# Optimization experiments

Hardware: AMD Instinct MI355X
Metric: run time of the kernel (lower is better)

Reference implementation:

```python
import jax, jax.numpy as jnp
import numpy as np
from jax import lax

EPS = 1e-5
S_CENTROIDS = 2048
K_NEIGH = 32


def _fps(xyz, S):
    """Farthest point sampling. xyz: (B,N,3) -> idx (B,S) int32."""
    B, N, _ = xyz.shape

    def body(carry, _):
        dist, farthest = carry  # (B,N), (B,)
        centroid = jnp.take_along_axis(xyz, farthest[:, None, None], axis=1)  # (B,1,3)
        d = jnp.sum((xyz - centroid) ** 2, axis=-1)  # (B,N)
        dist = jnp.minimum(dist, d)
        nxt = jnp.argmax(dist, axis=-1).astype(jnp.int32)
        return (dist, nxt), farthest

    init = (jnp.full((B, N), 1e10, xyz.dtype), jnp.zeros((B,), jnp.int32))
    _, idx = lax.scan(body, init, None, length=S)
    return idx.T  # (B,S)


def _knn(q, p, K):
    """q: (B,S,3) queries, p: (B,N,3) points -> idx (B,S,K) of K nearest."""
    d = (jnp.sum(q * q, -1)[:, :, None] + jnp.sum(p * p, -1)[:, None, :]
         - 2.0 * jnp.einsum('bsd,bnd->bsn', q, p))  # (B,S,N) sq dists
    _, idx = lax.top_k(-d, K)
    return idx


def _mlp_layer(x, w, g, b, m, v):
    # x: (B,S,K,Cin); 1x1 conv == channel matmul, then eval-mode BN, then ReLU
    x = jnp.einsum('bskc,oc->bsko', x, w)
    x = (x - m) * (g * lax.rsqrt(v + EPS)) + b
    return jax.nn.relu(x)


def setup_inputs() -> dict:
    key = jax.random.key(0)
    ks = jax.random.split(key, 8)
    B, N, D = 4, 8192, 64
    inp = {
        'xyz': jax.random.normal(ks[0], (B, N, 3), jnp.float32),
        'points': jax.random.normal(ks[1], (B, D, N), jnp.float32),
        'w0': jax.random.normal(ks[2], (64, 67), jnp.float32) * (1.0 / np.sqrt(67)),
        'g0': jnp.ones((64,), jnp.float32), 'b0': jnp.zeros((64,), jnp.float32),
        'm0': jnp.zeros((64,), jnp.float32), 'v0': jnp.ones((64,), jnp.float32),
        'w1': jax.random.normal(ks[3], (64, 64), jnp.float32) * (1.0 / np.sqrt(64)),
        'g1': jnp.ones((64,), jnp.float32), 'b1': jnp.zeros((64,), jnp.float32),
        'm1': jnp.zeros((64,), jnp.float32), 'v1': jnp.ones((64,), jnp.float32),
        'w2': jax.random.normal(ks[4], (128, 64), jnp.float32) * (1.0 / np.sqrt(64)),
        'g2': jnp.ones((128,), jnp.float32), 'b2': jnp.zeros((128,), jnp.float32),
        'm2': jnp.zeros((128,), jnp.float32), 'v2': jnp.ones((128,), jnp.float32),
    }
    return inp


def reference(xyz, points, w0, g0, b0, m0, v0, w1, g1, b1, m1, v1,
              w2, g2, b2, m2, v2):
    B, N, _ = xyz.shape
    S, K = S_CENTROIDS, K_NEIGH

    # FPS centroids (S < N path of the module)
    fps_idx = _fps(xyz, S)                                        # (B,S)
    new_xyz = jnp.take_along_axis(xyz, fps_idx[..., None], axis=1)  # (B,S,3)

    # KNN grouping
    idx = _knn(new_xyz, xyz, K)                                   # (B,S,K)
    grouped_xyz = jnp.take_along_axis(xyz[:, None], idx[..., None], axis=2)  # (B,S,K,3)
    grouped_xyz = grouped_xyz - new_xyz[:, :, None, :]

    # gather neighbor features: points (B,D,N) -> (B,N,D) -> (B,S,K,D)
    pts = jnp.transpose(points, (0, 2, 1))
    neigh = jnp.take_along_axis(pts[:, None], idx[..., None], axis=2)
    grouped = jnp.concatenate([grouped_xyz, neigh], axis=-1)      # (B,S,K,3+D)

    x = _mlp_layer(grouped, w0, g0, b0, m0, v0)
    x = _mlp_layer(x, w1, g1, b1, m1, v1)
    x = _mlp_layer(x, w2, g2, b2, m2, v2)                         # (B,S,K,128)

    new_points = jnp.transpose(jnp.max(x, axis=2), (0, 2, 1))     # (B,128,S)
    return new_xyz, new_points
```

## Files before the change

### kernel.cpp

```cpp
#include <hip/hip_runtime.h>
#include <cfloat>
#include <climits>

#define NPTS   8192
#define SCENT  2048
#define KNEIGH 32
#define BATCH  4
#define DFEAT  64
#define FPS_T  512
#define NV     8
#define NW     8
#define CAP    64
#define NCONS  252
#define CPB    63

typedef float v2f __attribute__((ext_vector_type(2)));

#define DPPMAX(u, ctrl, rmask)                                                        \
    { unsigned _t = (unsigned)__builtin_amdgcn_update_dpp(0, (int)(u), (ctrl),        \
                                                          (rmask), 0xf, false);      \
      (u) = ((u) > _t) ? (u) : _t; }

struct FpsSh {
    float sx[NPTS], sy[NPTS], sz[NPTS];
    float hx[SCENT], hy[SCENT], hz[SCENT];
    alignas(16) unsigned slotV[2][NW];
    alignas(16) unsigned slotM[2][NW];
    int scand[CAP];
    int scnt;
    alignas(8) double sdd[2][NW];
    double sfv[NW];
    int sfo[NW];
};
struct ConsSh {
    float  spx[2048], spy[2048], spz[2048];
    double sp2[2048];
    float  tile[32 * 33];
    float  regA[64 * 68];
    float  regB[64 * 64];
    float  regC[128 * 64];
    float  prm[512];
};
union ShU { FpsSh f; ConsSh c; };

__global__ __launch_bounds__(FPS_T, 1) void fused_kernel(
        const float* __restrict__ xyz, float* __restrict__ new_xyz,
        const float* __restrict__ pts, float* __restrict__ ptsT,
        int* __restrict__ progress, int* __restrict__ tcount,
        float* __restrict__ out_points,
        const float* __restrict__ w0, const float* __restrict__ g0,
        const float* __restrict__ b0, const float* __restrict__ m0,
        const float* __restrict__ v0, const float* __restrict__ w1,
        const float* __restrict__ g1, const float* __restrict__ b1,
        const float* __restrict__ m1, const float* __restrict__ v1,
        const float* __restrict__ w2, const float* __restrict__ g2,
        const float* __restrict__ b2, const float* __restrict__ m2,
        const float* __restrict__ v2) {
    __shared__ ShU sh;
    const int t = threadIdx.x;
    const int lane = t & 63, w = t >> 6;

    if (blockIdx.x < BATCH) {
        FpsSh& S = sh.f;
        const int b = blockIdx.x;
        const float* X = xyz + (size_t)b * NPTS * 3;

        for (int p = t; p < NPTS; p += FPS_T) {
            S.sx[p] = X[3 * p + 0]; S.sy[p] = X[3 * p + 1]; S.sz[p] = X[3 * p + 2];
        }

        v2f px2[NV], py2[NV], pz2[NV], dist2[NV];
#pragma unroll
        for (int j = 0; j < NV; ++j) {
            int pA = t + FPS_T * j, pB = t + FPS_T * (j + NV);
            px2[j] = (v2f){X[3 * pA + 0], X[3 * pB + 0]};
            py2[j] = (v2f){X[3 * pA + 1], X[3 * pB + 1]};
            pz2[j] = (v2f){X[3 * pA + 2], X[3 * pB + 2]};
            dist2[j] = (v2f){1e10f, 1e10f};
        }
        float cx = X[0], cy = X[1], cz = X[2];
        int buf = 0;
        __syncthreads();

#pragma unroll 1
        for (int s = 0; s < SCENT; ++s) {
            if (t == 0) { S.hx[s] = cx; S.hy[s] = cy; S.hz[s] = cz; }

            const v2f cxx = {cx, cx}, cyy = {cy, cy}, czz = {cz, cz};
            v2f m2 = {-1.f, -1.f}, s2 = {-1.f, -1.f};
#pragma unroll
            for (int j = 0; j < NV; ++j) {
                v2f dx = px2[j] - cxx;
                v2f dy = py2[j] - cyy;
                v2f dz = pz2[j] - czz;
                v2f d  = __builtin_elementwise_fma(dx, dx,
                         __builtin_elementwise_fma(dy, dy, dz * dz));
                v2f nd = __builtin_elementwise_min(dist2[j], d);
                dist2[j] = nd;
                v2f lo = __builtin_elementwise_min(m2, nd);
                s2 = __builtin_elementwise_max(s2, lo);
                m2 = __builtin_elementwise_max(m2, nd);
            }
            const float m   = fmaxf(m2.x, m2.y);
            const float sec = fmaxf(fmaxf(s2.x, s2.y), fminf(m2.x, m2.y));

            int mi = 0;
#pragma unroll
            for (int j = 0; j < NV; ++j) {
                mi = (dist2[j].x == m) ? (t + FPS_T * j)        : mi;
                mi = (dist2[j].y == m) ? (t + FPS_T * (j + NV)) : mi;
            }

            unsigned myU = __float_as_uint(m);
            unsigned u = myU;
            DPPMAX(u, 0x111, 0xf);
            DPPMAX(u, 0x112, 0xf);
            DPPMAX(u, 0x114, 0xf);
            DPPMAX(u, 0x118, 0xf);
            DPPMAX(u, 0x142, 0xa);
            DPPMAX(u, 0x143, 0xc);
            const unsigned wu = (unsigned)__builtin_amdgcn_readlane((int)u, 63);

            unsigned long long wb = __ballot(myU == wu);
            const int wl   = __ffsll(wb) - 1;
            const int widx = __builtin_amdgcn_readlane(mi, wl);
            const float thwf = __fmul_rn(__uint_as_float(wu), 0.999998f);
            unsigned long long b1m = __ballot(m >= thwf);
            unsigned long long b2m = __ballot(sec >= thwf);
            const unsigned tw = (b2m || __popcll(b1m) >= 2) ? 1u : 0u;
            if (lane == 0) {
                S.slotV[buf][w] = wu;
                S.slotM[buf][w] = (unsigned)widx | (tw << 14);
            }
            __syncthreads();

            unsigned sv[NW], sm[NW];
            {
                const uint4* vp = (const uint4*)&S.slotV[buf][0];
                const uint4* mp = (const uint4*)&S.slotM[buf][0];
                uint4 a = vp[0], c = vp[1], e = mp[0], f = mp[1];
                sv[0] = a.x; sv[1] = a.y; sv[2] = a.z; sv[3] = a.w;
                sv[4] = c.x; sv[5] = c.y; sv[6] = c.z; sv[7] = c.w;
                sm[0] = e.x; sm[1] = e.y; sm[2] = e.z; sm[3] = e.w;
                sm[4] = f.x; sm[5] = f.y; sm[6] = f.z; sm[7] = f.w;
            }
            unsigned gu = sv[0];
#pragma unroll
            for (int k = 1; k < NW; ++k) gu = (sv[k] > gu) ? sv[k] : gu;
            const float gvf  = __uint_as_float(gu);
            const float gthf = __fmul_rn(gvf, 0.999998f);
            const unsigned ugth = __float_as_uint(gthf);
            int nw = 0; unsigned meta = 0;
#pragma unroll
            for (int k = NW - 1; k >= 0; --k) {
                nw += (sv[k] >= ugth) ? 1 : 0;
                meta = (sv[k] == gu) ? sm[k] : meta;
            }
            const int wtie = (meta >> 14) & 1;
            int i1 = (int)(meta & 0x3fffu);

            if (nw >= 2 || wtie) {
                if (t == 0) S.scnt = 0;
                __syncthreads();
#pragma unroll
                for (int j = 0; j < NV; ++j) {
                    if (dist2[j].x >= gthf) {
                        int slot = atomicAdd(&S.scnt, 1);
                        if (slot < CAP) S.scand[slot] = t + FPS_T * j;
                    }
                    if (dist2[j].y >= gthf) {
                        int slot = atomicAdd(&S.scnt, 1);
                        if (slot < CAP) S.scand[slot] = t + FPS_T * (j + NV);
                    }
                }
                __syncthreads();
                const int mm = S.scnt;
                if (mm <= CAP) {
                    double bd = -1.0; int bi = INT_MAX;
#pragma unroll 1
                    for (int k = 0; k < mm; ++k) {
                        const int pos = S.scand[k];
                        const double pxd = (double)S.sx[pos], pyd = (double)S.sy[pos],
                                     pzd = (double)S.sz[pos];
                        double dd = 1e10;
                        for (int i = t; i <= s; i += FPS_T) {
                            double ddx = __dsub_rn(pxd, (double)S.hx[i]);
                            double ddy = __dsub_rn(pyd, (double)S.hy[i]);
                            double ddz = __dsub_rn(pzd, (double)S.hz[i]);
                            double d = __dadd_rn(__dadd_rn(__dmul_rn(ddx, ddx), __dmul_rn(ddy, ddy)),
                                                 __dmul_rn(ddz, ddz));
                            dd = fmin(dd, d);
                        }
#pragma unroll
                        for (int off = 32; off >= 1; off >>= 1)
                            dd = fmin(dd, __shfl_down(dd, off));
                        if (lane == 0) S.sdd[k & 1][w] = dd;
                        __syncthreads();
                        double ddm = S.sdd[k & 1][0];
#pragma unroll
                        for (int w2i = 1; w2i < NW; ++w2i) ddm = fmin(ddm, S.sdd[k & 1][w2i]);
                        if (ddm > bd || (ddm == bd && pos < bi)) { bd = ddm; bi = pos; }
                    }
                    i1 = bi;
                } else {
                    double bv = -1.0; int bi = INT_MAX;
#pragma unroll 1
                    for (int j = 0; j < 2 * NV; ++j) {
                        const int jj = j & (NV - 1);
                        const bool hiHalf = j >= NV;
                        const double pxd = (double)(hiHalf ? px2[jj].y : px2[jj].x);
                        const double pyd = (double)(hiHalf ? py2[jj].y : py2[jj].x);
                        const double pzd = (double)(hiHalf ? pz2[jj].y : pz2[jj].x);
                        double dd = 1e10;
                        for (int i = 0; i <= s; ++i) {
                            double ddx = __dsub_rn(pxd, (double)S.hx[i]);
                            double ddy = __dsub_rn(pyd, (double)S.hy[i]);
                            double ddz = __dsub_rn(pzd, (double)S.hz[i]);
                            double d = __dadd_rn(__dadd_rn(__dmul_rn(ddx, ddx), __dmul_rn(ddy, ddy)),
                                                 __dmul_rn(ddz, ddz));
                            dd = fmin(dd, d);
                        }
                        int pidx = t + FPS_T * j;
                        if (dd > bv || (dd == bv && pidx < bi)) { bv = dd; bi = pidx; }
                    }
#pragma unroll
                    for (int off = 32; off >= 1; off >>= 1) {
                        double ov = __shfl_down(bv, off);
                        int    oi = __shfl_down(bi, off);
                        if (ov > bv || (ov == bv && oi < bi)) { bv = ov; bi = oi; }
                    }
                    if (lane == 0) { S.sfv[w] = bv; S.sfo[w] = bi; }
                    __syncthreads();
                    bv = S.sfv[0]; bi = S.sfo[0];
#pragma unroll
                    for (int w2i = 1; w2i < NW; ++w2i) {
                        double ov = S.sfv[w2i]; int oi = S.sfo[w2i];
                        if (ov > bv || (ov == bv && oi < bi)) { bv = ov; bi = oi; }
                    }
                    i1 = bi;
                }
                __syncthreads();
            }
            cx = S.sx[i1]; cy = S.sy[i1]; cz = S.sz[i1];

            if ((s & 63) == 63) {
                const int base0 = s - 63;
                if (t < 64 * 3) {
                    int ci = base0 + t / 3;
                    int cmp = t - (t / 3) * 3;
                    float v = (cmp == 0) ? S.hx[ci] : ((cmp == 1) ? S.hy[ci] : S.hz[ci]);
                    __hip_atomic_store(&new_xyz[((size_t)b * SCENT + base0) * 3 + t], v,
                                       __ATOMIC_RELAXED, __HIP_MEMORY_SCOPE_AGENT);
                }
                __syncthreads();
                if (t == 0)
                    __hip_atomic_store(&progress[b], s + 1,
                                       __ATOMIC_RELEASE, __HIP_MEMORY_SCOPE_AGENT);
            }
            buf ^= 1;
        }
    } else {
        ConsSh& K = sh.c;
        const int local = blockIdx.x - BATCH;
        const int batch = local / CPB;
        const int cl    = local % CPB;
        const int tx = t & 31, ty = t >> 5;

        for (int tid2 = local; tid2 < 2048; tid2 += NCONS) {
            const int bt = tid2 >> 9, rest = tid2 & 511;
            const int d0 = (rest >> 8) * 32, n0 = (rest & 255) * 32;
            __syncthreads();
#pragma unroll
            for (int i = 0; i < 2; ++i)
                K.tile[(ty + 16 * i) * 33 + tx] =
                    pts[(size_t)bt * DFEAT * NPTS + (size_t)(d0 + ty + 16 * i) * NPTS + n0 + tx];
            __syncthreads();
#pragma unroll
            for (int i = 0; i < 2; ++i)
                ptsT[(size_t)bt * NPTS * DFEAT + (size_t)(n0 + ty + 16 * i) * DFEAT + d0 + tx] =
                    K.tile[tx * 33 + ty + 16 * i];
        }
        if (t == 0) {
            __threadfence();
            atomicAdd(tcount, 1);
        }

        for (int idx = t; idx < 64 * 68; idx += FPS_T) {
            int o = idx / 68, i = idx - o * 68;
            float v;
            if (i < 64)      v = w0[o * 67 + 3 + i];
            else if (i < 67) v = w0[o * 67 + (i - 64)];
            else             v = 0.0f;
            K.regA[idx] = v;
        }
        for (int idx = t; idx < 64 * 64; idx += FPS_T)  K.regB[idx] = w1[idx];
        for (int idx = t; idx < 128 * 64; idx += FPS_T) K.regC[idx] = w2[idx];
        if (t < 64) {
            float a0v = g0[t] / sqrtf(v0[t] + 1e-5f);
            K.prm[t]       = a0v;
            K.prm[64 + t]  = b0[t] - m0[t] * a0v;
            float a1v = g1[t] / sqrtf(v1[t] + 1e-5f);
            K.prm[128 + t] = a1v;
            K.prm[192 + t] = b1[t] - m1[t] * a1v;
        } else if (t < 192) {
            int o = t - 64;
            float a2v = g2[o] / sqrtf(v2[o] + 1e-5f);
            K.prm[256 + o] = a2v;
            K.prm[384 + o] = b2[o] - m2[o] * a2v;
        }

        const float* Xb = xyz + (size_t)batch * NPTS * 3;
#pragma unroll 1
        for (int r = 0; ; ++r) {
            const int sBase = r * (CPB * NW) + cl * NW;
            if (sBase >= SCENT) break;
            const int sMax = min(sBase + NW - 1, SCENT - 1);
            if (t == 0) {
                while (__hip_atomic_load(&progress[batch], __ATOMIC_ACQUIRE,
                                         __HIP_MEMORY_SCOPE_AGENT) < sMax + 1)
                    __builtin_amdgcn_s_sleep(8);
                if (r == 0) {
                    while (__hip_atomic_load(tcount, __ATOMIC_ACQUIRE,
                                             __HIP_MEMORY_SCOPE_AGENT) < NCONS)
                        __builtin_amdgcn_s_sleep(8);
                }
            }
            __syncthreads();

            const int sQ = min(sBase + w, SCENT - 1);
            const float* q = new_xyz + ((size_t)batch * SCENT + sQ) * 3;
            const float qfx = q[0], qfy = q[1], qfz = q[2];
            const double qx = (double)qfx, qy = (double)qfy, qz = (double)qfz;
            const double q2 = __dadd_rn(__dadd_rn(__dmul_rn(qx, qx), __dmul_rn(qy, qy)),
                                        __dmul_rn(qz, qz));

            double ld   = DBL_MAX;
            int    li   = 0x7fffffff;
            double taud = DBL_MAX;
            int    taui = 0x7fffffff;

#pragma unroll 1
            for (int c = 0; c < 4; ++c) {
                __syncthreads();
#pragma unroll
                for (int r2 = 0; r2 < 4; ++r2) {
                    int pl = r2 * 512 + t;
                    int p  = c * 2048 + pl;
                    float x = Xb[3 * p + 0], y = Xb[3 * p + 1], z = Xb[3 * p + 2];
                    K.spx[pl] = x; K.spy[pl] = y; K.spz[pl] = z;
                    double dx = (double)x, dy = (double)y, dz = (double)z;
                    K.sp2[pl] = __dadd_rn(__dadd_rn(__dmul_rn(dx, dx), __dmul_rn(dy, dy)),
                                          __dmul_rn(dz, dz));
                }
                __syncthreads();
#pragma unroll 1
                for (int i = 0; i < 32; ++i) {
                    const int pl   = i * 64 + lane;
                    const int pidx = c * 2048 + pl;
                    double px = (double)K.spx[pl], py = (double)K.spy[pl],
                           pz = (double)K.spz[pl];
                    double qp = __dadd_rn(__dadd_rn(__dmul_rn(qx, px), __dmul_rn(qy, py)),
                                          __dmul_rn(qz, pz));
                    double d  = __dsub_rn(__dadd_rn(q2, K.sp2[pl]), __dmul_rn(2.0, qp));
                    bool cand = (d < taud) || (d == taud && pidx < taui);
                    unsigned long long mmask = __ballot(cand);
                    while (mmask) {
                        int sl = __ffsll((unsigned long long)mmask) - 1;
                        mmask &= mmask - 1;
                        double dv = __shfl(d, sl);
                        int    iv = __shfl(pidx, sl);
                        if (dv < taud || (dv == taud && iv < taui)) {
                            bool gt = (lane < 32) && (ld > dv || (ld == dv && li > iv));
                            unsigned long long gm = __ballot(gt);
                            double ud = __shfl_up(ld, 1);
                            int    ui = __shfl_up(li, 1);
                            if (gt) { ld = ud; li = ui; }
                            bool first = gt && ((lane == 0) || !((gm >> (lane - 1)) & 1ull));
                            if (first) { ld = dv; li = iv; }
                            taud = __shfl(ld, 31);
                            taui = __shfl(li, 31);
                        }
                    }
                }
            }

            if (sBase + w < SCENT && lane < 32) {
                const int nidx = li;
                const float* P3 = Xb + (size_t)nidx * 3;
                const float dx = P3[0] - qfx, dy = P3[1] - qfy, dz = P3[2] - qfz;

                const float4* F = (const float4*)(ptsT + ((size_t)batch * NPTS + nidx) * 64);
                float4 xv[17];
#pragma unroll
                for (int i = 0; i < 16; ++i) xv[i] = F[i];
                xv[16] = make_float4(dx, dy, dz, 0.0f);

                float h0[64];
                const float4* W0 = (const float4*)K.regA;
#pragma unroll
                for (int o = 0; o < 64; ++o) {
                    float acc = 0.f;
#pragma unroll
                    for (int i = 0; i < 17; ++i) {
                        float4 ww = W0[o * 17 + i];
                        acc = fmaf(xv[i].x, ww.x, acc);
                        acc = fmaf(xv[i].y, ww.y, acc);
                        acc = fmaf(xv[i].z, ww.z, acc);
                        acc = fmaf(xv[i].w, ww.w, acc);
                    }
                    h0[o] = fmaxf(fmaf(acc, K.prm[o], K.prm[64 + o]), 0.f);
                }
                float h1[64];
                const float4* W1 = (const float4*)K.regB;
#pragma unroll
                for (int o = 0; o < 64; ++o) {
                    float acc = 0.f;
#pragma unroll
                    for (int i = 0; i < 16; ++i) {
                        float4 ww = W1[o * 16 + i];
                        acc = fmaf(h0[4 * i + 0], ww.x, acc);
                        acc = fmaf(h0[4 * i + 1], ww.y, acc);
                        acc = fmaf(h0[4 * i + 2], ww.z, acc);
                        acc = fmaf(h0[4 * i + 3], ww.w, acc);
                    }
                    h1[o] = fmaxf(fmaf(acc, K.prm[128 + o], K.prm[192 + o]), 0.f);
                }
                const float4* W2 = (const float4*)K.regC;
                float* outp = out_points + (size_t)batch * 128 * SCENT + sQ;
#pragma unroll 1
                for (int o = 0; o < 128; ++o) {
                    float acc = 0.f;
#pragma unroll
                    for (int i = 0; i < 16; ++i) {
                        float4 ww = W2[o * 16 + i];
                        acc = fmaf(h1[4 * i + 0], ww.x, acc);
                        acc = fmaf(h1[4 * i + 1], ww.y, acc);
                        acc = fmaf(h1[4 * i + 2], ww.z, acc);
                        acc = fmaf(h1[4 * i + 3], ww.w, acc);
                    }
                    float y = fmaxf(fmaf(acc, K.prm[256 + o], K.prm[384 + o]), 0.f);
#pragma unroll
                    for (int off = 16; off >= 1; off >>= 1)
                        y = fmaxf(y, __shfl_xor(y, off));
                    if (lane == 0) outp[(size_t)o * SCENT] = y;
                }
            }
        }
    }
}

extern "C" void kernel_launch(void* const* d_in, const int* in_sizes, int n_in,
                              void* d_out, int out_size, void* d_ws, size_t ws_size,
                              hipStream_t stream) {
    const float* xyz    = (const float*)d_in[0];
    const float* points = (const float*)d_in[1];
    const float* w0 = (const float*)d_in[2];
    const float* g0 = (const float*)d_in[3];
    const float* b0 = (const float*)d_in[4];
    const float* m0 = (const float*)d_in[5];
    const float* v0 = (const float*)d_in[6];
    const float* w1 = (const float*)d_in[7];
    const float* g1 = (const float*)d_in[8];
    const float* b1 = (const float*)d_in[9];
    const float* m1 = (const float*)d_in[10];
    const float* v1 = (const float*)d_in[11];
    const float* w2 = (const float*)d_in[12];
    const float* g2 = (const float*)d_in[13];
    const float* b2 = (const float*)d_in[14];
    const float* m2 = (const float*)d_in[15];
    const float* v2 = (const float*)d_in[16];

    float* out_xyz    = (float*)d_out;
    float* out_points = (float*)d_out + (size_t)BATCH * SCENT * 3;

    char* ws = (char*)d_ws;
    int*   progress = (int*)ws;
    int*   tcount   = (int*)(ws + 64);
    float* ptsT     = (float*)(ws + 32768);

    hipMemsetAsync(ws, 0, 128, stream);

    void* kargs[] = { (void*)&xyz, (void*)&out_xyz, (void*)&points, (void*)&ptsT,
                      (void*)&progress, (void*)&tcount, (void*)&out_points,
                      (void*)&w0, (void*)&g0, (void*)&b0, (void*)&m0, (void*)&v0,
                      (void*)&w1, (void*)&g1, (void*)&b1, (void*)&m1, (void*)&v1,
                      (void*)&w2, (void*)&g2, (void*)&b2, (void*)&m2, (void*)&v2 };
    hipLaunchCooperativeKernel((const void*)fused_kernel,
                               dim3(BATCH + NCONS), dim3(FPS_T), kargs, 0, stream);
}
```

Measured before the change: 2.484 ms.

## Speculatively select two FPS centroids per iteration using per-wave top-2 reduction

Each wave now reduces both its maximum and its second-largest distance through the DPP network, and publishes both. When the global runner-up comes from a different wave and is provably far enough from the chosen centroid that the new centroid cannot change its distance, the next centroid is accepted without another pass and block barrier. The following distance update then applies both centroids in a single fused loop. This aims to halve the number of serial FPS iterations and barriers, at the cost of extra reduction work, more register use, and correctness that depends on the safety conditions being tight.

```diff
diff --git a/kernel.cpp b/kernel.cpp
--- a/kernel.cpp
+++ b/kernel.cpp
@@ -16,16 +16,42 @@
 
 typedef float v2f __attribute__((ext_vector_type(2)));
 
-#define DPPMAX(u, ctrl, rmask)                                                        \
-    { unsigned _t = (unsigned)__builtin_amdgcn_update_dpp(0, (int)(u), (ctrl),        \
-                                                          (rmask), 0xf, false);      \
-      (u) = ((u) > _t) ? (u) : _t; }
+#define DPPTOP2(um, us, ctrl, rmask)                                                  \
+    { unsigned _tm = (unsigned)__builtin_amdgcn_update_dpp(0, (int)(um), (ctrl),      \
+                                                           (rmask), 0xf, false);     \
+      unsigned _ts = (unsigned)__builtin_amdgcn_update_dpp(0, (int)(us), (ctrl),      \
+                                                           (rmask), 0xf, false);     \
+      unsigned _lo = ((um) < _tm) ? (um) : _tm;                                       \
+      (us) = ((us) > _ts) ? (us) : _ts;                                               \
+      (us) = ((us) > _lo) ? (us) : _lo;                                               \
+      (um) = ((um) > _tm) ? (um) : _tm; }
+
+#define FLUSH_PUB(Eidx, VX, VY, VZ, HASPREV, PX, PY, PZ)                              \
+    if (((Eidx) & 63) == 63) {                                                        \
+        const int base0 = (Eidx) - 63;                                                \
+        if (t < 64 * 3) {                                                             \
+            const int ci = base0 + t / 3;                                             \
+            const int cc = t - (t / 3) * 3;                                           \
+            float v;                                                                  \
+            if (ci == (Eidx))                                                         \
+                v = (cc == 0) ? (VX) : ((cc == 1) ? (VY) : (VZ));                     \
+            else if ((HASPREV) && ci == (Eidx) - 1)                                   \
+                v = (cc == 0) ? (PX) : ((cc == 1) ? (PY) : (PZ));                     \
+            else                                                                      \
+                v = (cc == 0) ? S.hx[ci] : ((cc == 1) ? S.hy[ci] : S.hz[ci]);         \
+            __hip_atomic_store(&new_xyz[((size_t)b * SCENT + base0) * 3 + t], v,      \
+                               __ATOMIC_RELAXED, __HIP_MEMORY_SCOPE_AGENT);           \
+        }                                                                             \
+        __syncthreads();                 \
+        if (t == 0)                                                                   \
+            __hip_atomic_store(&progress[b], (Eidx) + 1,                              \
+                               __ATOMIC_RELEASE, __HIP_MEMORY_SCOPE_AGENT);           \
+    }
 
 struct FpsSh {
     float sx[NPTS], sy[NPTS], sz[NPTS];
     float hx[SCENT], hy[SCENT], hz[SCENT];
-    alignas(16) unsigned slotV[2][NW];
-    alignas(16) unsigned slotM[2][NW];
+    alignas(16) unsigned slotQ[2][NW][4];
     int scand[CAP];
     int scnt;
     alignas(8) double sdd[2][NW];
@@ -78,31 +104,50 @@
             pz2[j] = (v2f){X[3 * pA + 2], X[3 * pB + 2]};
             dist2[j] = (v2f){1e10f, 1e10f};
         }
-        float cx = X[0], cy = X[1], cz = X[2];
-        int buf = 0;
+        float c0x = X[0], c0y = X[1], c0z = X[2];
+        float c1x = 0.f, c1y = 0.f, c1z = 0.f;
+        int dual = 0, buf = 0;
+        int E = 1;
+        if (t == 0) { S.hx[0] = c0x; S.hy[0] = c0y; S.hz[0] = c0z; }
         __syncthreads();
 
 #pragma unroll 1
-        for (int s = 0; s < SCENT; ++s) {
-            if (t == 0) { S.hx[s] = cx; S.hy[s] = cy; S.hz[s] = cz; }
-
-            const v2f cxx = {cx, cx}, cyy = {cy, cy}, czz = {cz, cz};
-            v2f m2 = {-1.f, -1.f}, s2 = {-1.f, -1.f};
-#pragma unroll
-            for (int j = 0; j < NV; ++j) {
-                v2f dx = px2[j] - cxx;
-                v2f dy = py2[j] - cyy;
-                v2f dz = pz2[j] - czz;
-                v2f d  = __builtin_elementwise_fma(dx, dx,
-                         __builtin_elementwise_fma(dy, dy, dz * dz));
-                v2f nd = __builtin_elementwise_min(dist2[j], d);
-                dist2[j] = nd;
-                v2f lo = __builtin_elementwise_min(m2, nd);
-                s2 = __builtin_elementwise_max(s2, lo);
-                m2 = __builtin_elementwise_max(m2, nd);
-            }
-            const float m   = fmaxf(m2.x, m2.y);
-            const float sec = fmaxf(fmaxf(s2.x, s2.y), fminf(m2.x, m2.y));
+        while (true) {
+            float m2s = -1.f, s2s = -1.f;
+            {
+                const v2f c0xx = {c0x, c0x}, c0yy = {c0y, c0y}, c0zz = {c0z, c0z};
+                if (dual) {
+                    const v2f c1xx = {c1x, c1x}, c1yy = {c1y, c1y}, c1zz = {c1z, c1z};
+#pragma unroll
+                    for (int j = 0; j < NV; ++j) {
+                        v2f dx = px2[j] - c0xx, dy = py2[j] - c0yy, dz = pz2[j] - c0zz;
+                        v2f d0 = __builtin_elementwise_fma(dx, dx,
+                                 __builtin_elementwise_fma(dy, dy, dz * dz));
+                        v2f ex = px2[j] - c1xx, ey = py2[j] - c1yy, ez = pz2[j] - c1zz;
+                        v2f d1 = __builtin_elementwise_fma(ex, ex,
+                                 __builtin_elementwise_fma(ey, ey, ez * ez));
+                        v2f d  = __builtin_elementwise_min(d0, d1);
+                        v2f nd = __builtin_elementwise_min(dist2[j], d);
+                        dist2[j] = nd;
+                        float hi = fmaxf(nd.x, nd.y), lo = fminf(nd.x, nd.y);
+                        s2s = fmaxf(fmaxf(s2s, lo), fminf(m2s, hi));
+                        m2s = fmaxf(m2s, hi);
+                    }
+                } else {
+#pragma unroll
+                    for (int j = 0; j < NV; ++j) {
+                        v2f dx = px2[j] - c0xx, dy = py2[j] - c0yy, dz = pz2[j] - c0zz;
+                        v2f d  = __builtin_elementwise_fma(dx, dx,
+                                 __builtin_elementwise_fma(dy, dy, dz * dz));
+                        v2f nd = __builtin_elementwise_min(dist2[j], d);
+                        dist2[j] = nd;
+                        float hi = fmaxf(nd.x, nd.y), lo = fminf(nd.x, nd.y);
+                        s2s = fmaxf(fmaxf(s2s, lo), fminf(m2s, hi));
+                        m2s = fmaxf(m2s, hi);
+                    }
+                }
+            }
+            const float m = m2s, sec = s2s;
 
             int mi = 0;
 #pragma unroll
@@ -111,15 +156,16 @@
                 mi = (dist2[j].y == m) ? (t + FPS_T * (j + NV)) : mi;
             }
 
-            unsigned myU = __float_as_uint(m);
-            unsigned u = myU;
-            DPPMAX(u, 0x111, 0xf);
-            DPPMAX(u, 0x112, 0xf);
-            DPPMAX(u, 0x114, 0xf);
-            DPPMAX(u, 0x118, 0xf);
-            DPPMAX(u, 0x142, 0xa);
-            DPPMAX(u, 0x143, 0xc);
-            const unsigned wu = (unsigned)__builtin_amdgcn_readlane((int)u, 63);
+            const unsigned myU = __float_as_uint(m);
+            unsigned um = myU, us = __float_as_uint(sec);
+            DPPTOP2(um, us, 0x111, 0xf);
+            DPPTOP2(um, us, 0x112, 0xf);
+            DPPTOP2(um, us, 0x114, 0xf);
+            DPPTOP2(um, us, 0x118, 0xf);
+            DPPTOP2(um, us, 0x142, 0xa);
+            DPPTOP2(um, us, 0x143, 0xc);
+            const unsigned wu  = (unsigned)__builtin_amdgcn_readlane((int)um, 63);
+            const unsigned wsu = (unsigned)__builtin_amdgcn_readlane((int)us, 63);
 
             unsigned long long wb = __ballot(myU == wu);
             const int wl   = __ffsll(wb) - 1;
@@ -129,37 +175,43 @@
             unsigned long long b2m = __ballot(sec >= thwf);
             const unsigned tw = (b2m || __popcll(b1m) >= 2) ? 1u : 0u;
             if (lane == 0) {
-                S.slotV[buf][w] = wu;
-                S.slotM[buf][w] = (unsigned)widx | (tw << 14);
+                *(uint4*)&S.slotQ[buf][w][0] =
+                    make_uint4(wu, (unsigned)widx | (tw << 14), wsu, 0u);
             }
             __syncthreads();
 
-            unsigned sv[NW], sm[NW];
+            unsigned mv[NW], mt4[NW], sv2[NW];
             {
-                const uint4* vp = (const uint4*)&S.slotV[buf][0];
-                const uint4* mp = (const uint4*)&S.slotM[buf][0];
-                uint4 a = vp[0], c = vp[1], e = mp[0], f = mp[1];
-                sv[0] = a.x; sv[1] = a.y; sv[2] = a.z; sv[3] = a.w;
-                sv[4] = c.x; sv[5] = c.y; sv[6] = c.z; sv[7] = c.w;
-                sm[0] = e.x; sm[1] = e.y; sm[2] = e.z; sm[3] = e.w;
-                sm[4] = f.x; sm[5] = f.y; sm[6] = f.z; sm[7] = f.w;
-            }
-            unsigned gu = sv[0];
-#pragma unroll
-            for (int k = 1; k < NW; ++k) gu = (sv[k] > gu) ? sv[k] : gu;
+                const uint4* qp = (const uint4*)&S.slotQ[buf][0][0];
+                uint4 u0 = qp[0], u1 = qp[1], u2 = qp[2], u3 = qp[3];
+                uint4 u4 = qp[4], u5 = qp[5], u6 = qp[6], u7 = qp[7];
+                mv[0]=u0.x; mt4[0]=u0.y; sv2[0]=u0.z;
+                mv[1]=u1.x; mt4[1]=u1.y; sv2[1]=u1.z;
+                mv[2]=u2.x; mt4[2]=u2.y; sv2[2]=u2.z;
+                mv[3]=u3.x; mt4[3]=u3.y; sv2[3]=u3.z;
+                mv[4]=u4.x; mt4[4]=u4.y; sv2[4]=u4.z;
+                mv[5]=u5.x; mt4[5]=u5.y; sv2[5]=u5.z;
+                mv[6]=u6.x; mt4[6]=u6.y; sv2[6]=u6.z;
+                mv[7]=u7.x; mt4[7]=u7.y; sv2[7]=u7.z;
+            }
+            unsigned gu = mv[0];
+#pragma unroll
+            for (int k = 1; k < NW; ++k) gu = (mv[k] > gu) ? mv[k] : gu;
             const float gvf  = __uint_as_float(gu);
             const float gthf = __fmul_rn(gvf, 0.999998f);
             const unsigned ugth = __float_as_uint(gthf);
-            int nw = 0; unsigned meta = 0;
+            int nw = 0; unsigned meta = 0; int kw = 0;
 #pragma unroll
             for (int k = NW - 1; k >= 0; --k) {
-                nw += (sv[k] >= ugth) ? 1 : 0;
-                meta = (sv[k] == gu) ? sm[k] : meta;
+                nw  += (mv[k] >= ugth) ? 1 : 0;
+                meta = (mv[k] == gu) ? mt4[k] : meta;
+                kw   = (mv[k] == gu) ? k : kw;
             }
             const int wtie = (meta >> 14) & 1;
             int i1 = (int)(meta & 0x3fffu);
-
-            if (nw >= 2 || wtie) {
+            const int fb = (nw >= 2) || wtie;
+
+            if (fb) {
                 if (t == 0) S.scnt = 0;
                 __syncthreads();
 #pragma unroll
@@ -183,7 +235,7 @@
                         const double pxd = (double)S.sx[pos], pyd = (double)S.sy[pos],
                                      pzd = (double)S.sz[pos];
                         double dd = 1e10;
-                        for (int i = t; i <= s; i += FPS_T) {
+                        for (int i = t; i < E; i += FPS_T) {
                             double ddx = __dsub_rn(pxd, (double)S.hx[i]);
                             double ddy = __dsub_rn(pyd, (double)S.hy[i]);
                             double ddz = __dsub_rn(pzd, (double)S.hz[i]);
@@ -212,7 +264,7 @@
                         const double pyd = (double)(hiHalf ? py2[jj].y : py2[jj].x);
                         const double pzd = (double)(hiHalf ? pz2[jj].y : pz2[jj].x);
                         double dd = 1e10;
-                        for (int i = 0; i <= s; ++i) {
+                        for (int i = 0; i < E; ++i) {
                             double ddx = __dsub_rn(pxd, (double)S.hx[i]);
                             double ddy = __dsub_rn(pyd, (double)S.hy[i]);
                             double ddz = __dsub_rn(pzd, (double)S.hz[i]);
@@ -241,22 +293,52 @@
                 }
                 __syncthreads();
             }
-            cx = S.sx[i1]; cy = S.sy[i1]; cz = S.sz[i1];
-
-            if ((s & 63) == 63) {
-                const int base0 = s - 63;
-                if (t < 64 * 3) {
-                    int ci = base0 + t / 3;
-                    int cmp = t - (t / 3) * 3;
-                    float v = (cmp == 0) ? S.hx[ci] : ((cmp == 1) ? S.hy[ci] : S.hz[ci]);
-                    __hip_atomic_store(&new_xyz[((size_t)b * SCENT + base0) * 3 + t], v,
-                                       __ATOMIC_RELAXED, __HIP_MEMORY_SCOPE_AGENT);
-                }
-                __syncthreads();
-                if (t == 0)
-                    __hip_atomic_store(&progress[b], s + 1,
-                                       __ATOMIC_RELEASE, __HIP_MEMORY_SCOPE_AGENT);
-            }
+
+            const float e0x = S.sx[i1], e0y = S.sy[i1], e0z = S.sz[i1];
+            if (t == 0) { S.hx[E] = e0x; S.hy[E] = e0y; S.hz[E] = e0z; }
+            FLUSH_PUB(E, e0x, e0y, e0z, 0, 0.f, 0.f, 0.f);
+            c0x = e0x; c0y = e0y; c0z = e0z;
+
+            int peeled = 0;
+            float e1x = 0.f, e1y = 0.f, e1z = 0.f;
+            if (!fb && (E + 1) < SCENT) {
+                unsigned arr[NW];
+#pragma unroll
+                for (int k = 0; k < NW; ++k) arr[k] = (k == kw) ? sv2[k] : mv[k];
+                unsigned v2u = arr[0];
+#pragma unroll
+                for (int k = 1; k < NW; ++k) v2u = (arr[k] > v2u) ? arr[k] : v2u;
+                int k2 = 0; unsigned meta2 = 0;
+#pragma unroll
+                for (int k = NW - 1; k >= 0; --k) {
+                    meta2 = (arr[k] == v2u) ? mt4[k] : meta2;
+                    k2    = (arr[k] == v2u) ? k : k2;
+                }
+                const float v2vf = __uint_as_float(v2u);
+                const unsigned uthr2 = __float_as_uint(__fmul_rn(v2vf, 0.999998f));
+                int cnt = 0;
+#pragma unroll
+                for (int k = 0; k < NW; ++k)
+                    cnt += ((mv[k] >= uthr2) ? 1 : 0) + ((sv2[k] >= uthr2) ? 1 : 0);
+                const int i2 = (int)(meta2 & 0x3fffu);
+                e1x = S.sx[i2]; e1y = S.sy[i2]; e1z = S.sz[i2];
+                const float ddx = e1x - e0x, ddy = e1y - e0y, ddz = e1z - e0z;
+                const float dq = fmaf(ddx, ddx, fmaf(ddy, ddy, ddz * ddz));
+                peeled = ((k2 != kw) && (cnt == 2) &&
+                          (dq >= __fmul_rn(v2vf, 1.000002f))) ? 1 : 0;
+            }
+            if (peeled) {
+                const int e1i = E + 1;
+                if (t == 0) { S.hx[e1i] = e1x; S.hy[e1i] = e1y; S.hz[e1i] = e1z; }
+                FLUSH_PUB(e1i, e1x, e1y, e1z, 1, e0x, e0y, e0z);
+                c1x = e1x; c1y = e1y; c1z = e1z;
+                dual = 1;
+                E = e1i + 1;
+            } else {
+                dual = 0;
+                E = E + 1;
+            }
+            if (E >= SCENT) break;
             buf ^= 1;
         }
     } else {
```

New measurement: 2.332 ms. 1.07x faster.
